# Kernel tuning notes

Hardware: AMD Instinct MI355X
Metric: run time of the kernel (lower is better)

Reference implementation:

```python
import jax, jax.numpy as jnp
import numpy as np

EPS = 1e-5
K = 7            # involution kernel size
GC = 16          # group_channels (involution default)
RED = 4          # reduction ratio (involution default)


def _bn(x, g, b, m, v):
    # eval-mode BatchNorm2d over channel dim of NCHW
    scale = g / jnp.sqrt(v + EPS)
    return x * scale[None, :, None, None] + (b - m * scale)[None, :, None, None]


def setup_inputs() -> dict:
    key = jax.random.key(0)
    ks = jax.random.split(key, 24)
    C_in, C_out = 64, 128
    B, H, W = 4, 96, 96
    G = C_in // GC          # 4 involution groups
    Cr = C_in // RED        # 16 reduced channels

    def bn_params(k, c):
        k1, k2, k3, k4 = jax.random.split(k, 4)
        return (jax.random.uniform(k1, (c,)) + 0.5,          # gamma
                jax.random.normal(k2, (c,)) * 0.1,            # beta
                jax.random.normal(k3, (c,)) * 0.1,            # running mean
                jax.random.uniform(k4, (c,)) + 0.5)           # running var

    g_r, b_r, m_r, v_r = bn_params(ks[1], Cr)
    g_i, b_i, m_i, v_i = bn_params(ks[2], C_in)
    g_c, b_c, m_c, v_c = bn_params(ks[3], C_out)
    g_m, b_m, m_m, v_m = bn_params(ks[4], C_out)

    return {
        "x": jax.random.normal(ks[0], (B, C_in, H, W), dtype=jnp.float32),
        "w_reduce": jax.random.normal(ks[5], (Cr, C_in), dtype=jnp.float32) * 0.1,
        "g_r": g_r, "b_r": b_r, "m_r": m_r, "v_r": v_r,
        "w_span": jax.random.normal(ks[6], (K * K * G, Cr), dtype=jnp.float32) * 0.1,
        "b_span": jax.random.normal(ks[7], (K * K * G,), dtype=jnp.float32) * 0.1,
        "g_i": g_i, "b_i": b_i, "m_i": m_i, "v_i": v_i,
        "w_conv": jax.random.normal(ks[8], (C_out, C_in), dtype=jnp.float32) * 0.1,
        "g_c": g_c, "b_c": b_c, "m_c": m_c, "v_c": v_c,
        "w_map": jax.random.normal(ks[9], (C_out, C_in), dtype=jnp.float32) * 0.1,
        "b_map": jax.random.normal(ks[10], (C_out,), dtype=jnp.float32) * 0.1,
        "g_m": g_m, "b_m": b_m, "m_m": m_m, "v_m": v_m,
    }


def reference(x, w_reduce, g_r, b_r, m_r, v_r, w_span, b_span,
              g_i, b_i, m_i, v_i, w_conv, g_c, b_c, m_c, v_c,
              w_map, b_map, g_m, b_m, m_m, v_m):
    B, C, H, W = x.shape
    G = C // GC
    pad = (K - 1) // 2

    # --- Involution: dynamic per-pixel kernels ---
    t = jax.nn.relu(_bn(jnp.einsum('rc,bchw->brhw', w_reduce, x), g_r, b_r, m_r, v_r))
    kern = jnp.einsum('or,brhw->bohw', w_span, t) + b_span[None, :, None, None]
    kern = kern.reshape(B, G, 1, K * K, H, W)  # [B,G,1,KK,H,W]

    xp = jnp.pad(x, ((0, 0), (0, 0), (pad, pad), (pad, pad)))
    # unfold in torch (C, kh, kw) order: C slowest -> stack over kernel offsets
    patches = jnp.stack([xp[:, :, i:i + H, j:j + W]
                         for i in range(K) for j in range(K)], axis=2)  # [B,C,KK,H,W]
    patches = patches.reshape(B, G, GC, K * K, H, W)
    inv = (kern * patches).sum(axis=3).reshape(B, C, H, W)

    # --- BN + GELU, 1x1 conv + BN, mapping branch, residual + GELU ---
    x1 = jax.nn.gelu(_bn(inv, g_i, b_i, m_i, v_i), approximate=False)
    x1 = _bn(jnp.einsum('oc,bchw->bohw', w_conv, x1), g_c, b_c, m_c, v_c)
    xm = _bn(jnp.einsum('oc,bchw->bohw', w_map, x) + b_map[None, :, None, None],
             g_m, b_m, m_m, v_m)
    return jax.nn.gelu(x1 + xm, approximate=False)
```

## Files before the change

kernel.cpp:

```cpp
#include <hip/hip_runtime.h>
#include <hip/hip_bf16.h>
#include <math.h>

typedef __hip_bfloat16 bf16;
typedef __attribute__((ext_vector_type(8))) short v8s;
typedef __attribute__((ext_vector_type(4))) short v4s;
typedef __attribute__((ext_vector_type(4))) float v4f;

#define HD 96
#define WD 96
#define HW 9216
#define BATCH 4

#define OFF_WR    0
#define OFF_CR    1024
#define OFF_WSP   1040
#define OFF_BSP   4176
#define OFF_SI    4372
#define OFF_CI    4436
#define OFF_BIAS  4500
#define WFRAG_BYTE 18512
#define ZT_BYTE   51328

__device__ __forceinline__ float geluf(float v) {
    return 0.5f * v * (1.0f + erff(v * 0.7071067811865475f));
}

__global__ __launch_bounds__(256) void k_fold(
    const float* __restrict__ wred,
    const float* __restrict__ gr, const float* __restrict__ br,
    const float* __restrict__ mr, const float* __restrict__ vr,
    const float* __restrict__ wspan, const float* __restrict__ bspan,
    const float* __restrict__ gi, const float* __restrict__ bi,
    const float* __restrict__ mi, const float* __restrict__ vi,
    const float* __restrict__ wconv,
    const float* __restrict__ gc, const float* __restrict__ bc,
    const float* __restrict__ mc, const float* __restrict__ vc,
    const float* __restrict__ wmap, const float* __restrict__ bmap,
    const float* __restrict__ gm, const float* __restrict__ bm,
    const float* __restrict__ mmn, const float* __restrict__ vm,
    float* __restrict__ wsf, bf16* __restrict__ wfrag)
{
    const int gt = blockIdx.x * 256 + threadIdx.x;

    if (gt < 1024) {
        int r = gt >> 6;
        float sr = gr[r] * rsqrtf(vr[r] + 1e-5f);
        wsf[OFF_WR + gt] = sr * wred[gt];
    }
    if (gt < 16) {
        float sr = gr[gt] * rsqrtf(vr[gt] + 1e-5f);
        wsf[OFF_CR + gt] = br[gt] - mr[gt] * sr;
    }
    if (gt < 3136) wsf[OFF_WSP + gt] = wspan[gt];
    if (gt < 196)  wsf[OFF_BSP + gt] = bspan[gt];
    if (gt < 64) {
        float si = gi[gt] * rsqrtf(vi[gt] + 1e-5f);
        wsf[OFF_SI + gt] = si;
        wsf[OFF_CI + gt] = bi[gt] - mi[gt] * si;
    }
    if (gt < 128) {
        float sc = gc[gt] * rsqrtf(vc[gt] + 1e-5f);
        float sm = gm[gt] * rsqrtf(vm[gt] + 1e-5f);
        wsf[OFF_BIAS + gt] = (bc[gt] - mc[gt] * sc)
                           + sm * bmap[gt]
                           + (bm[gt] - mmn[gt] * sm);
    }
    {
        int j    = gt & 7;
        int lane = (gt >> 3) & 63;
        int ks   = (gt >> 9) & 3;
        int mt   = gt >> 11;
        int m = mt * 16 + (lane & 15);
        int k = ks * 32 + (lane >> 4) * 8 + j;
        float v;
        if (k < 64) {
            float sc = gc[m] * rsqrtf(vc[m] + 1e-5f);
            v = sc * wconv[m * 64 + k];
        } else {
            float sm = gm[m] * rsqrtf(vm[m] + 1e-5f);
            v = sm * wmap[m * 64 + (k - 64)];
        }
        wfrag[gt] = __float2bfloat16(v);
    }
}

__global__ __launch_bounds__(256) void k_inv2(
    const float* __restrict__ x, const float* __restrict__ wsf,
    bf16* __restrict__ zt)
{
    __shared__ float xs4[3136];
    __shared__ float ks[49 * 64];
    __shared__ float ts[64 * 17];

    const int tid = threadIdx.x;
    const int bz  = blockIdx.z;
    const int b   = bz >> 2, g = bz & 3;
    const int ty  = blockIdx.y * 8, tx = blockIdx.x * 8;

    const float* xb = x + (size_t)b * 64 * HW;

    for (int it = tid; it < 784; it += 256) {
        int qc = it / 196, pos = it % 196;
        int py = pos / 14, px = pos % 14;
        int gy = ty + py - 3, gx = tx + px - 3;
        v4f v = (v4f){0.f, 0.f, 0.f, 0.f};
        if (gy >= 0 && gy < HD && gx >= 0 && gx < WD) {
            const float* pp = xb + (size_t)(g * 16 + qc * 4) * HW + gy * WD + gx;
            v[0] = pp[0]; v[1] = pp[HW]; v[2] = pp[2 * HW]; v[3] = pp[3 * HW];
        }
        *(v4f*)&xs4[it * 4] = v;
    }

    const int p  = tid & 63;
    const int u  = __builtin_amdgcn_readfirstlane(tid >> 6);
    const int py0 = p >> 3, px0 = p & 7;
    const int hw  = (ty + py0) * WD + (tx + px0);

    float t4[4];
    #pragma unroll
    for (int r = 0; r < 4; ++r) t4[r] = wsf[OFF_CR + u * 4 + r];
    #pragma unroll 4
    for (int c = 0; c < 64; ++c) {
        float xc = xb[(size_t)c * HW + hw];
        #pragma unroll
        for (int r = 0; r < 4; ++r)
            t4[r] += wsf[OFF_WR + (u * 4 + r) * 64 + c] * xc;
    }
    #pragma unroll
    for (int r = 0; r < 4; ++r) ts[p * 17 + u * 4 + r] = fmaxf(t4[r], 0.0f);
    __syncthreads();

    float tr[16];
    #pragma unroll
    for (int r = 0; r < 16; ++r) tr[r] = ts[p * 17 + r];

    for (int kk = u; kk < 49; kk += 4) {
        int row = g * 49 + kk;
        float kv = wsf[OFF_BSP + row];
        #pragma unroll
        for (int r = 0; r < 16; ++r) kv += wsf[OFF_WSP + row * 16 + r] * tr[r];
        ks[kk * 64 + p] = kv;
    }
    __syncthreads();

    float acc[4] = {0.f, 0.f, 0.f, 0.f};
    #pragma unroll 1
    for (int i = 0; i < 7; ++i) {
        const int rowb = (py0 + i) * 14 + px0;
        #pragma unroll
        for (int j = 0; j < 7; ++j) {
            float kv = ks[(i * 7 + j) * 64 + p];
            v4f xv = *(const v4f*)&xs4[(u * 196 + rowb + j) * 4];
            acc[0] += kv * xv[0];
            acc[1] += kv * xv[1];
            acc[2] += kv * xv[2];
            acc[3] += kv * xv[3];
        }
    }

    const int c0 = g * 16 + u * 4;
    bf16* ztr = zt + ((size_t)b * HW + hw) * 128;

    v4s pk1;
    #pragma unroll
    for (int ci = 0; ci < 4; ++ci) {
        float v = acc[ci] * wsf[OFF_SI + c0 + ci] + wsf[OFF_CI + c0 + ci];
        pk1[ci] = (short)__bfloat16_as_ushort(__float2bfloat16(geluf(v)));
    }
    *(v4s*)&ztr[c0] = pk1;

    const int center = (py0 + 3) * 14 + (px0 + 3);
    v4f xc = *(const v4f*)&xs4[(u * 196 + center) * 4];
    v4s pk2;
    #pragma unroll
    for (int ci = 0; ci < 4; ++ci)
        pk2[ci] = (short)__bfloat16_as_ushort(__float2bfloat16(xc[ci]));
    *(v4s*)&ztr[64 + c0] = pk2;
}

__global__ __launch_bounds__(256) void k_out2(
    const bf16* __restrict__ zt, const float* __restrict__ wsf,
    const bf16* __restrict__ wfrag, float* __restrict__ out)
{
    const int tid  = threadIdx.x;
    const int lane = tid & 63;
    const int wv   = tid >> 6;
    const int n    = lane & 15;
    const int quad = lane >> 4;

    const int pxg = blockIdx.x * 64 + wv * 16 + n;
    const int b   = pxg / HW;
    const int hw  = pxg % HW;

    const v8s* zb = (const v8s*)(zt + (size_t)pxg * 128);
    v8s bfr[4];
    #pragma unroll
    for (int ks = 0; ks < 4; ++ks) bfr[ks] = zb[ks * 4 + quad];

    const v8s* wf = (const v8s*)wfrag;
    v4f acc[8];
    #pragma unroll
    for (int mt = 0; mt < 8; ++mt) acc[mt] = (v4f){0.f, 0.f, 0.f, 0.f};

    #pragma unroll
    for (int ks = 0; ks < 4; ++ks) {
        #pragma unroll
        for (int mt = 0; mt < 8; ++mt) {
            v8s afrag = wf[(mt * 4 + ks) * 64 + lane];
            acc[mt] = __builtin_amdgcn_mfma_f32_16x16x32_bf16(afrag, bfr[ks], acc[mt], 0, 0, 0);
        }
    }

    #pragma unroll
    for (int mt = 0; mt < 8; ++mt) {
        int m0 = mt * 16 + quad * 4;
        v4f bs = *(const v4f*)&wsf[OFF_BIAS + m0];
        #pragma unroll
        for (int reg = 0; reg < 4; ++reg) {
            float v = acc[mt][reg] + bs[reg];
            out[((size_t)(b * 128 + m0 + reg)) * HW + hw] = geluf(v);
        }
    }
}

extern "C" void kernel_launch(void* const* d_in, const int* in_sizes, int n_in,
                              void* d_out, int out_size, void* d_ws, size_t ws_size,
                              hipStream_t stream)
{
    const float* x     = (const float*)d_in[0];
    const float* wred  = (const float*)d_in[1];
    const float* gr    = (const float*)d_in[2];
    const float* br    = (const float*)d_in[3];
    const float* mr    = (const float*)d_in[4];
    const float* vr    = (const float*)d_in[5];
    const float* wspan = (const float*)d_in[6];
    const float* bspan = (const float*)d_in[7];
    const float* gi    = (const float*)d_in[8];
    const float* bi    = (const float*)d_in[9];
    const float* mi    = (const float*)d_in[10];
    const float* vi    = (const float*)d_in[11];
    const float* wconv = (const float*)d_in[12];
    const float* gc    = (const float*)d_in[13];
    const float* bc    = (const float*)d_in[14];
    const float* mc    = (const float*)d_in[15];
    const float* vc    = (const float*)d_in[16];
    const float* wmap  = (const float*)d_in[17];
    const float* bmap  = (const float*)d_in[18];
    const float* gm    = (const float*)d_in[19];
    const float* bm    = (const float*)d_in[20];
    const float* mmn   = (const float*)d_in[21];
    const float* vm    = (const float*)d_in[22];

    float* wsf   = (float*)d_ws;
    bf16*  wfrag = (bf16*)((char*)d_ws + WFRAG_BYTE);
    bf16*  zt    = (bf16*)((char*)d_ws + ZT_BYTE);
    float* out   = (float*)d_out;

    hipLaunchKernelGGL(k_fold, dim3(64), dim3(256), 0, stream,
                       wred, gr, br, mr, vr, wspan, bspan, gi, bi, mi, vi,
                       wconv, gc, bc, mc, vc, wmap, bmap, gm, bm, mmn, vm,
                       wsf, wfrag);
    hipLaunchKernelGGL(k_inv2, dim3(12, 12, 16), dim3(256), 0, stream, x, wsf, zt);
    hipLaunchKernelGGL(k_out2, dim3((BATCH * HW) / 64), dim3(256), 0, stream,
                       zt, wsf, wfrag, out);
}
```

Measured before the change: 159.2 us.

## Fuse involution and output GEMM into one kernel with bf16 LDS halo

Merges the involution kernel and the MFMA output kernel into a single kernel, so each block handles a 16x4 pixel tile across all 4 groups and keeps the bf16 intermediate in shared memory. This removes the global round-trip of the 128-channel intermediate and one launch. The input halo for all 64 channels is now stored in LDS as bf16, which cuts LDS footprint but rounds the input to bf16 before the reduce conv and the involution. The grid shrinks to 576 blocks, each with more serialized work and more syncs, and the 16-wide tile has a larger halo overhead.

```diff
diff --git a/kernel.cpp b/kernel.cpp
--- a/kernel.cpp
+++ b/kernel.cpp
@@ -11,6 +11,13 @@
 #define WD 96
 #define HW 9216
 #define BATCH 4
+
+#define TW 16
+#define TH 4
+#define HALO_W 22
+#define HALO_H 10
+#define NPOS 220
+#define ZLS 136
 
 #define OFF_WR    0
 #define OFF_CR    1024
@@ -20,10 +27,21 @@
 #define OFF_CI    4436
 #define OFF_BIAS  4500
 #define WFRAG_BYTE 18512
-#define ZT_BYTE   51328
 
 __device__ __forceinline__ float geluf(float v) {
     return 0.5f * v * (1.0f + erff(v * 0.7071067811865475f));
+}
+__device__ __forceinline__ v4f up4(v4s s) {
+    v4f r;
+    #pragma unroll
+    for (int i = 0; i < 4; ++i) {
+        unsigned int uu = ((unsigned int)(unsigned short)s[i]) << 16;
+        r[i] = __builtin_bit_cast(float, uu);
+    }
+    return r;
+}
+__device__ __forceinline__ short pkbf(float f) {
+    return (short)__bfloat16_as_ushort(__float2bfloat16(f));
 }
 
 __global__ __launch_bounds__(256) void k_fold(
@@ -85,140 +103,140 @@
     }
 }
 
-__global__ __launch_bounds__(256) void k_inv2(
+__global__ __launch_bounds__(256) void k_main(
     const float* __restrict__ x, const float* __restrict__ wsf,
-    bf16* __restrict__ zt)
+    const bf16* __restrict__ wfrag, float* __restrict__ out)
 {
-    __shared__ float xs4[3136];
-    __shared__ float ks[49 * 64];
+    __shared__ v4s   xh4[16 * NPOS];
+    __shared__ float ksh[49 * 64];
     __shared__ float ts[64 * 17];
+    __shared__ short zl[64 * ZLS];
 
     const int tid = threadIdx.x;
-    const int bz  = blockIdx.z;
-    const int b   = bz >> 2, g = bz & 3;
-    const int ty  = blockIdx.y * 8, tx = blockIdx.x * 8;
+    const int b   = blockIdx.z;
+    const int ty  = blockIdx.y * TH;
+    const int tx  = blockIdx.x * TW;
 
     const float* xb = x + (size_t)b * 64 * HW;
 
-    for (int it = tid; it < 784; it += 256) {
-        int qc = it / 196, pos = it % 196;
-        int py = pos / 14, px = pos % 14;
+    for (int it = tid; it < 16 * NPOS; it += 256) {
+        int cb = it / NPOS, pos = it % NPOS;
+        int py = pos / HALO_W, px = pos % HALO_W;
         int gy = ty + py - 3, gx = tx + px - 3;
-        v4f v = (v4f){0.f, 0.f, 0.f, 0.f};
+        v4s v = (v4s){0, 0, 0, 0};
         if (gy >= 0 && gy < HD && gx >= 0 && gx < WD) {
-            const float* pp = xb + (size_t)(g * 16 + qc * 4) * HW + gy * WD + gx;
-            v[0] = pp[0]; v[1] = pp[HW]; v[2] = pp[2 * HW]; v[3] = pp[3 * HW];
-        }
-        *(v4f*)&xs4[it * 4] = v;
-    }
+            const float* pp = xb + (size_t)(cb * 4) * HW + gy * WD + gx;
+            v[0] = pkbf(pp[0]);
+            v[1] = pkbf(pp[HW]);
+            v[2] = pkbf(pp[2 * HW]);
+            v[3] = pkbf(pp[3 * HW]);
+        }
+        xh4[it] = v;
+    }
+    __syncthreads();
 
     const int p  = tid & 63;
     const int u  = __builtin_amdgcn_readfirstlane(tid >> 6);
-    const int py0 = p >> 3, px0 = p & 7;
-    const int hw  = (ty + py0) * WD + (tx + px0);
+    const int py0 = p >> 4, px0 = p & 15;
+    const int center = (py0 + 3) * HALO_W + (px0 + 3);
 
     float t4[4];
     #pragma unroll
     for (int r = 0; r < 4; ++r) t4[r] = wsf[OFF_CR + u * 4 + r];
-    #pragma unroll 4
-    for (int c = 0; c < 64; ++c) {
-        float xc = xb[(size_t)c * HW + hw];
-        #pragma unroll
-        for (int r = 0; r < 4; ++r)
-            t4[r] += wsf[OFF_WR + (u * 4 + r) * 64 + c] * xc;
+    #pragma unroll
+    for (int cb = 0; cb < 16; ++cb) {
+        v4f xf = up4(xh4[cb * NPOS + center]);
+        #pragma unroll
+        for (int ci = 0; ci < 4; ++ci) {
+            #pragma unroll
+            for (int r = 0; r < 4; ++r)
+                t4[r] += wsf[OFF_WR + (u * 4 + r) * 64 + cb * 4 + ci] * xf[ci];
+        }
     }
     #pragma unroll
     for (int r = 0; r < 4; ++r) ts[p * 17 + u * 4 + r] = fmaxf(t4[r], 0.0f);
+
+    #pragma unroll
+    for (int m = 0; m < 4; ++m) {
+        int cb = m * 4 + u;
+        *(v4s*)&zl[p * ZLS + 64 + cb * 4] = xh4[cb * NPOS + center];
+    }
     __syncthreads();
 
     float tr[16];
     #pragma unroll
     for (int r = 0; r < 16; ++r) tr[r] = ts[p * 17 + r];
 
-    for (int kk = u; kk < 49; kk += 4) {
-        int row = g * 49 + kk;
-        float kv = wsf[OFF_BSP + row];
-        #pragma unroll
-        for (int r = 0; r < 16; ++r) kv += wsf[OFF_WSP + row * 16 + r] * tr[r];
-        ks[kk * 64 + p] = kv;
-    }
-    __syncthreads();
-
-    float acc[4] = {0.f, 0.f, 0.f, 0.f};
-    #pragma unroll 1
-    for (int i = 0; i < 7; ++i) {
-        const int rowb = (py0 + i) * 14 + px0;
-        #pragma unroll
-        for (int j = 0; j < 7; ++j) {
-            float kv = ks[(i * 7 + j) * 64 + p];
-            v4f xv = *(const v4f*)&xs4[(u * 196 + rowb + j) * 4];
-            acc[0] += kv * xv[0];
-            acc[1] += kv * xv[1];
-            acc[2] += kv * xv[2];
-            acc[3] += kv * xv[3];
-        }
-    }
-
-    const int c0 = g * 16 + u * 4;
-    bf16* ztr = zt + ((size_t)b * HW + hw) * 128;
-
-    v4s pk1;
-    #pragma unroll
-    for (int ci = 0; ci < 4; ++ci) {
-        float v = acc[ci] * wsf[OFF_SI + c0 + ci] + wsf[OFF_CI + c0 + ci];
-        pk1[ci] = (short)__bfloat16_as_ushort(__float2bfloat16(geluf(v)));
-    }
-    *(v4s*)&ztr[c0] = pk1;
-
-    const int center = (py0 + 3) * 14 + (px0 + 3);
-    v4f xc = *(const v4f*)&xs4[(u * 196 + center) * 4];
-    v4s pk2;
-    #pragma unroll
-    for (int ci = 0; ci < 4; ++ci)
-        pk2[ci] = (short)__bfloat16_as_ushort(__float2bfloat16(xc[ci]));
-    *(v4s*)&ztr[64 + c0] = pk2;
-}
-
-__global__ __launch_bounds__(256) void k_out2(
-    const bf16* __restrict__ zt, const float* __restrict__ wsf,
-    const bf16* __restrict__ wfrag, float* __restrict__ out)
-{
-    const int tid  = threadIdx.x;
+    for (int g = 0; g < 4; ++g) {
+        for (int kk = u; kk < 49; kk += 4) {
+            int row = g * 49 + kk;
+            float kv = wsf[OFF_BSP + row];
+            #pragma unroll
+            for (int r = 0; r < 16; ++r) kv += wsf[OFF_WSP + row * 16 + r] * tr[r];
+            ksh[kk * 64 + p] = kv;
+        }
+        __syncthreads();
+
+        const int cb = g * 4 + u;
+        float acc[4] = {0.f, 0.f, 0.f, 0.f};
+        #pragma unroll 1
+        for (int i = 0; i < 7; ++i) {
+            const int rowb = (py0 + i) * HALO_W + px0;
+            #pragma unroll
+            for (int j = 0; j < 7; ++j) {
+                float kv = ksh[(i * 7 + j) * 64 + p];
+                v4f xv = up4(xh4[cb * NPOS + rowb + j]);
+                acc[0] += kv * xv[0];
+                acc[1] += kv * xv[1];
+                acc[2] += kv * xv[2];
+                acc[3] += kv * xv[3];
+            }
+        }
+
+        const int c0 = cb * 4;
+        v4s pk;
+        #pragma unroll
+        for (int ci = 0; ci < 4; ++ci) {
+            float v = acc[ci] * wsf[OFF_SI + c0 + ci] + wsf[OFF_CI + c0 + ci];
+            pk[ci] = pkbf(geluf(v));
+        }
+        *(v4s*)&zl[p * ZLS + c0] = pk;
+        __syncthreads();
+    }
+
     const int lane = tid & 63;
-    const int wv   = tid >> 6;
     const int n    = lane & 15;
     const int quad = lane >> 4;
-
-    const int pxg = blockIdx.x * 64 + wv * 16 + n;
-    const int b   = pxg / HW;
-    const int hw  = pxg % HW;
-
-    const v8s* zb = (const v8s*)(zt + (size_t)pxg * 128);
+    const int wv   = tid >> 6;
+    const int pxl  = wv * 16 + n;
+
     v8s bfr[4];
     #pragma unroll
-    for (int ks = 0; ks < 4; ++ks) bfr[ks] = zb[ks * 4 + quad];
+    for (int ki = 0; ki < 4; ++ki)
+        bfr[ki] = *(const v8s*)&zl[pxl * ZLS + ki * 32 + quad * 8];
 
     const v8s* wf = (const v8s*)wfrag;
-    v4f acc[8];
-    #pragma unroll
-    for (int mt = 0; mt < 8; ++mt) acc[mt] = (v4f){0.f, 0.f, 0.f, 0.f};
-
-    #pragma unroll
-    for (int ks = 0; ks < 4; ++ks) {
+    v4f acc2[8];
+    #pragma unroll
+    for (int mt = 0; mt < 8; ++mt) acc2[mt] = (v4f){0.f, 0.f, 0.f, 0.f};
+
+    #pragma unroll
+    for (int ki = 0; ki < 4; ++ki) {
         #pragma unroll
         for (int mt = 0; mt < 8; ++mt) {
-            v8s afrag = wf[(mt * 4 + ks) * 64 + lane];
-            acc[mt] = __builtin_amdgcn_mfma_f32_16x16x32_bf16(afrag, bfr[ks], acc[mt], 0, 0, 0);
-        }
-    }
-
+            v8s afrag = wf[(mt * 4 + ki) * 64 + lane];
+            acc2[mt] = __builtin_amdgcn_mfma_f32_16x16x32_bf16(afrag, bfr[ki], acc2[mt], 0, 0, 0);
+        }
+    }
+
+    const int hw = (ty + wv) * WD + tx + n;
     #pragma unroll
     for (int mt = 0; mt < 8; ++mt) {
         int m0 = mt * 16 + quad * 4;
         v4f bs = *(const v4f*)&wsf[OFF_BIAS + m0];
         #pragma unroll
         for (int reg = 0; reg < 4; ++reg) {
-            float v = acc[mt][reg] + bs[reg];
+            float v = acc2[mt][reg] + bs[reg];
             out[((size_t)(b * 128 + m0 + reg)) * HW + hw] = geluf(v);
         }
     }
@@ -254,14 +272,12 @@
 
     float* wsf   = (float*)d_ws;
     bf16*  wfrag = (bf16*)((char*)d_ws + WFRAG_BYTE);
-    bf16*  zt    = (bf16*)((char*)d_ws + ZT_BYTE);
     float* out   = (float*)d_out;
 
     hipLaunchKernelGGL(k_fold, dim3(64), dim3(256), 0, stream,
                        wred, gr, br, mr, vr, wspan, bspan, gi, bi, mi, vi,
                        wconv, gc, bc, mc, vc, wmap, bmap, gm, bm, mmn, vm,
                        wsf, wfrag);
-    hipLaunchKernelGGL(k_inv2, dim3(12, 12, 16), dim3(256), 0, stream, x, wsf, zt);
-    hipLaunchKernelGGL(k_out2, dim3((BATCH * HW) / 64), dim3(256), 0, stream,
-                       zt, wsf, wfrag, out);
-}
+    hipLaunchKernelGGL(k_main, dim3(WD / TW, HD / TH, BATCH), dim3(256), 0, stream,
+                       x, wsf, wfrag, out);
+}
```

Result: slower. 180.3 us (+13.2%).

## Precompute reduce-conv activations once per pixel and split output GEMM across waves

Applied to the files above, without the earlier changes.

The reduce 1x1 conv (64->16 channels plus BN and ReLU) was previously recomputed in every involution block, once for each of the 4 groups. It is now computed once per pixel in a new stage fused into the weight-folding kernel and stored as bf16. The involution kernel reads these 16 values instead of re-reading all 64 input channels. The output kernel now gives each wave 2 of the 8 M-tiles for 16 pixels instead of all 8 tiles for its own pixels, which means more blocks and fewer accumulators per thread. The cost is an extra bf16 round trip through global memory and a small loss of precision on the reduced activations.

```diff
diff --git a/kernel.cpp b/kernel.cpp
--- a/kernel.cpp
+++ b/kernel.cpp
@@ -11,6 +11,7 @@
 #define WD 96
 #define HW 9216
 #define BATCH 4
+#define NPIX (BATCH * HW)
 
 #define OFF_WR    0
 #define OFF_CR    1024
@@ -20,13 +21,22 @@
 #define OFF_CI    4436
 #define OFF_BIAS  4500
 #define WFRAG_BYTE 18512
-#define ZT_BYTE   51328
+#define TG_BYTE   51328
+#define ZT_BYTE   1230976
 
 __device__ __forceinline__ float geluf(float v) {
     return 0.5f * v * (1.0f + erff(v * 0.7071067811865475f));
 }
-
-__global__ __launch_bounds__(256) void k_fold(
+__device__ __forceinline__ float upbf(short s) {
+    unsigned int uu = ((unsigned int)(unsigned short)s) << 16;
+    return __builtin_bit_cast(float, uu);
+}
+__device__ __forceinline__ short pkbf(float f) {
+    return (short)__bfloat16_as_ushort(__float2bfloat16(f));
+}
+
+__global__ __launch_bounds__(256) void k_pre(
+    const float* __restrict__ x,
     const float* __restrict__ wred,
     const float* __restrict__ gr, const float* __restrict__ br,
     const float* __restrict__ mr, const float* __restrict__ vr,
@@ -39,59 +49,98 @@
     const float* __restrict__ wmap, const float* __restrict__ bmap,
     const float* __restrict__ gm, const float* __restrict__ bm,
     const float* __restrict__ mmn, const float* __restrict__ vm,
-    float* __restrict__ wsf, bf16* __restrict__ wfrag)
+    float* __restrict__ wsf, bf16* __restrict__ wfrag, bf16* __restrict__ tg)
 {
-    const int gt = blockIdx.x * 256 + threadIdx.x;
-
-    if (gt < 1024) {
-        int r = gt >> 6;
-        float sr = gr[r] * rsqrtf(vr[r] + 1e-5f);
-        wsf[OFF_WR + gt] = sr * wred[gt];
-    }
-    if (gt < 16) {
-        float sr = gr[gt] * rsqrtf(vr[gt] + 1e-5f);
-        wsf[OFF_CR + gt] = br[gt] - mr[gt] * sr;
-    }
-    if (gt < 3136) wsf[OFF_WSP + gt] = wspan[gt];
-    if (gt < 196)  wsf[OFF_BSP + gt] = bspan[gt];
-    if (gt < 64) {
-        float si = gi[gt] * rsqrtf(vi[gt] + 1e-5f);
-        wsf[OFF_SI + gt] = si;
-        wsf[OFF_CI + gt] = bi[gt] - mi[gt] * si;
-    }
-    if (gt < 128) {
-        float sc = gc[gt] * rsqrtf(vc[gt] + 1e-5f);
-        float sm = gm[gt] * rsqrtf(vm[gt] + 1e-5f);
-        wsf[OFF_BIAS + gt] = (bc[gt] - mc[gt] * sc)
-                           + sm * bmap[gt]
-                           + (bm[gt] - mmn[gt] * sm);
-    }
-    {
-        int j    = gt & 7;
-        int lane = (gt >> 3) & 63;
-        int ks   = (gt >> 9) & 3;
-        int mt   = gt >> 11;
-        int m = mt * 16 + (lane & 15);
-        int k = ks * 32 + (lane >> 4) * 8 + j;
-        float v;
-        if (k < 64) {
-            float sc = gc[m] * rsqrtf(vc[m] + 1e-5f);
-            v = sc * wconv[m * 64 + k];
-        } else {
-            float sm = gm[m] * rsqrtf(vm[m] + 1e-5f);
-            v = sm * wmap[m * 64 + (k - 64)];
-        }
-        wfrag[gt] = __float2bfloat16(v);
-    }
-}
-
-__global__ __launch_bounds__(256) void k_inv2(
+    const int tid = threadIdx.x;
+    const int blk = blockIdx.x;
+
+    if (blk < 64) {
+        const int gt = blk * 256 + tid;
+        if (gt < 1024) {
+            int r = gt >> 6;
+            float sr = gr[r] * rsqrtf(vr[r] + 1e-5f);
+            wsf[OFF_WR + gt] = sr * wred[gt];
+        }
+        if (gt < 16) {
+            float sr = gr[gt] * rsqrtf(vr[gt] + 1e-5f);
+            wsf[OFF_CR + gt] = br[gt] - mr[gt] * sr;
+        }
+        if (gt < 3136) wsf[OFF_WSP + gt] = wspan[gt];
+        if (gt < 196)  wsf[OFF_BSP + gt] = bspan[gt];
+        if (gt < 64) {
+            float si = gi[gt] * rsqrtf(vi[gt] + 1e-5f);
+            wsf[OFF_SI + gt] = si;
+            wsf[OFF_CI + gt] = bi[gt] - mi[gt] * si;
+        }
+        if (gt < 128) {
+            float sc = gc[gt] * rsqrtf(vc[gt] + 1e-5f);
+            float sm = gm[gt] * rsqrtf(vm[gt] + 1e-5f);
+            wsf[OFF_BIAS + gt] = (bc[gt] - mc[gt] * sc)
+                               + sm * bmap[gt]
+                               + (bm[gt] - mmn[gt] * sm);
+        }
+        {
+            int j    = gt & 7;
+            int lane = (gt >> 3) & 63;
+            int ks   = (gt >> 9) & 3;
+            int mt   = gt >> 11;
+            int m = mt * 16 + (lane & 15);
+            int k = ks * 32 + (lane >> 4) * 8 + j;
+            float v;
+            if (k < 64) {
+                float sc = gc[m] * rsqrtf(vc[m] + 1e-5f);
+                v = sc * wconv[m * 64 + k];
+            } else {
+                float sm = gm[m] * rsqrtf(vm[m] + 1e-5f);
+                v = sm * wmap[m * 64 + (k - 64)];
+            }
+            wfrag[gt] = __float2bfloat16(v);
+        }
+        return;
+    }
+
+    __shared__ float wrl[1024];
+    __shared__ float crl[16];
+    for (int i = tid; i < 1024; i += 256) {
+        int r = i >> 6;
+        wrl[i] = gr[r] * rsqrtf(vr[r] + 1e-5f) * wred[i];
+    }
+    if (tid < 16)
+        crl[tid] = br[tid] - mr[tid] * gr[tid] * rsqrtf(vr[tid] + 1e-5f);
+    __syncthreads();
+
+    const int p = tid & 63, u = tid >> 6;
+    const int gpix = (blk - 64) * 64 + p;
+    const int b = gpix / HW, hw = gpix % HW;
+    const float* xb = x + (size_t)b * 64 * HW + hw;
+
+    float t4[4];
+    #pragma unroll
+    for (int r = 0; r < 4; ++r) t4[r] = crl[u * 4 + r];
+    #pragma unroll 4
+    for (int c4 = 0; c4 < 16; ++c4) {
+        float xc0 = xb[(size_t)(c4 * 4 + 0) * HW];
+        float xc1 = xb[(size_t)(c4 * 4 + 1) * HW];
+        float xc2 = xb[(size_t)(c4 * 4 + 2) * HW];
+        float xc3 = xb[(size_t)(c4 * 4 + 3) * HW];
+        #pragma unroll
+        for (int r = 0; r < 4; ++r) {
+            v4f w = *(const v4f*)&wrl[(u * 4 + r) * 64 + c4 * 4];
+            t4[r] += w[0] * xc0 + w[1] * xc1 + w[2] * xc2 + w[3] * xc3;
+        }
+    }
+    v4s pk;
+    #pragma unroll
+    for (int r = 0; r < 4; ++r) pk[r] = pkbf(fmaxf(t4[r], 0.0f));
+    *(v4s*)((short*)tg + (size_t)gpix * 16 + u * 4) = pk;
+}
+
+__global__ __launch_bounds__(256) void k_inv3(
     const float* __restrict__ x, const float* __restrict__ wsf,
-    bf16* __restrict__ zt)
+    const bf16* __restrict__ tg, bf16* __restrict__ zt)
 {
     __shared__ float xs4[3136];
-    __shared__ float ks[49 * 64];
-    __shared__ float ts[64 * 17];
+    __shared__ float ksh[49 * 64];
 
     const int tid = threadIdx.x;
     const int bz  = blockIdx.z;
@@ -116,31 +165,20 @@
     const int u  = __builtin_amdgcn_readfirstlane(tid >> 6);
     const int py0 = p >> 3, px0 = p & 7;
     const int hw  = (ty + py0) * WD + (tx + px0);
-
-    float t4[4];
-    #pragma unroll
-    for (int r = 0; r < 4; ++r) t4[r] = wsf[OFF_CR + u * 4 + r];
-    #pragma unroll 4
-    for (int c = 0; c < 64; ++c) {
-        float xc = xb[(size_t)c * HW + hw];
-        #pragma unroll
-        for (int r = 0; r < 4; ++r)
-            t4[r] += wsf[OFF_WR + (u * 4 + r) * 64 + c] * xc;
-    }
-    #pragma unroll
-    for (int r = 0; r < 4; ++r) ts[p * 17 + u * 4 + r] = fmaxf(t4[r], 0.0f);
-    __syncthreads();
-
+    const int gpix = b * HW + hw;
+
+    const v8s* tp = (const v8s*)((const short*)tg + (size_t)gpix * 16);
+    v8s t01 = tp[0], t23 = tp[1];
     float tr[16];
     #pragma unroll
-    for (int r = 0; r < 16; ++r) tr[r] = ts[p * 17 + r];
+    for (int i = 0; i < 8; ++i) { tr[i] = upbf(t01[i]); tr[8 + i] = upbf(t23[i]); }
 
     for (int kk = u; kk < 49; kk += 4) {
         int row = g * 49 + kk;
         float kv = wsf[OFF_BSP + row];
         #pragma unroll
         for (int r = 0; r < 16; ++r) kv += wsf[OFF_WSP + row * 16 + r] * tr[r];
-        ks[kk * 64 + p] = kv;
+        ksh[kk * 64 + p] = kv;
     }
     __syncthreads();
 
@@ -150,7 +188,7 @@
         const int rowb = (py0 + i) * 14 + px0;
         #pragma unroll
         for (int j = 0; j < 7; ++j) {
-            float kv = ks[(i * 7 + j) * 64 + p];
+            float kv = ksh[(i * 7 + j) * 64 + p];
             v4f xv = *(const v4f*)&xs4[(u * 196 + rowb + j) * 4];
             acc[0] += kv * xv[0];
             acc[1] += kv * xv[1];
@@ -166,7 +204,7 @@
     #pragma unroll
     for (int ci = 0; ci < 4; ++ci) {
         float v = acc[ci] * wsf[OFF_SI + c0 + ci] + wsf[OFF_CI + c0 + ci];
-        pk1[ci] = (short)__bfloat16_as_ushort(__float2bfloat16(geluf(v)));
+        pk1[ci] = pkbf(geluf(v));
     }
     *(v4s*)&ztr[c0] = pk1;
 
@@ -174,51 +212,51 @@
     v4f xc = *(const v4f*)&xs4[(u * 196 + center) * 4];
     v4s pk2;
     #pragma unroll
-    for (int ci = 0; ci < 4; ++ci)
-        pk2[ci] = (short)__bfloat16_as_ushort(__float2bfloat16(xc[ci]));
+    for (int ci = 0; ci < 4; ++ci) pk2[ci] = pkbf(xc[ci]);
     *(v4s*)&ztr[64 + c0] = pk2;
 }
 
-__global__ __launch_bounds__(256) void k_out2(
+__global__ __launch_bounds__(256) void k_out3(
     const bf16* __restrict__ zt, const float* __restrict__ wsf,
     const bf16* __restrict__ wfrag, float* __restrict__ out)
 {
     const int tid  = threadIdx.x;
     const int lane = tid & 63;
-    const int wv   = tid >> 6;
+    const int mq   = tid >> 6;
     const int n    = lane & 15;
     const int quad = lane >> 4;
 
-    const int pxg = blockIdx.x * 64 + wv * 16 + n;
+    const int pxg = blockIdx.x * 16 + n;
     const int b   = pxg / HW;
     const int hw  = pxg % HW;
 
     const v8s* zb = (const v8s*)(zt + (size_t)pxg * 128);
     v8s bfr[4];
     #pragma unroll
-    for (int ks = 0; ks < 4; ++ks) bfr[ks] = zb[ks * 4 + quad];
+    for (int ki = 0; ki < 4; ++ki) bfr[ki] = zb[ki * 4 + quad];
 
     const v8s* wf = (const v8s*)wfrag;
-    v4f acc[8];
-    #pragma unroll
-    for (int mt = 0; mt < 8; ++mt) acc[mt] = (v4f){0.f, 0.f, 0.f, 0.f};
-
-    #pragma unroll
-    for (int ks = 0; ks < 4; ++ks) {
-        #pragma unroll
-        for (int mt = 0; mt < 8; ++mt) {
-            v8s afrag = wf[(mt * 4 + ks) * 64 + lane];
-            acc[mt] = __builtin_amdgcn_mfma_f32_16x16x32_bf16(afrag, bfr[ks], acc[mt], 0, 0, 0);
-        }
-    }
-
-    #pragma unroll
-    for (int mt = 0; mt < 8; ++mt) {
-        int m0 = mt * 16 + quad * 4;
+    v4f acc[2];
+    acc[0] = (v4f){0.f, 0.f, 0.f, 0.f};
+    acc[1] = (v4f){0.f, 0.f, 0.f, 0.f};
+
+    #pragma unroll
+    for (int ki = 0; ki < 4; ++ki) {
+        #pragma unroll
+        for (int m = 0; m < 2; ++m) {
+            int mt = mq * 2 + m;
+            v8s afrag = wf[(mt * 4 + ki) * 64 + lane];
+            acc[m] = __builtin_amdgcn_mfma_f32_16x16x32_bf16(afrag, bfr[ki], acc[m], 0, 0, 0);
+        }
+    }
+
+    #pragma unroll
+    for (int m = 0; m < 2; ++m) {
+        int m0 = (mq * 2 + m) * 16 + quad * 4;
         v4f bs = *(const v4f*)&wsf[OFF_BIAS + m0];
         #pragma unroll
         for (int reg = 0; reg < 4; ++reg) {
-            float v = acc[mt][reg] + bs[reg];
+            float v = acc[m][reg] + bs[reg];
             out[((size_t)(b * 128 + m0 + reg)) * HW + hw] = geluf(v);
         }
     }
@@ -254,14 +292,16 @@
 
     float* wsf   = (float*)d_ws;
     bf16*  wfrag = (bf16*)((char*)d_ws + WFRAG_BYTE);
+    bf16*  tg    = (bf16*)((char*)d_ws + TG_BYTE);
     bf16*  zt    = (bf16*)((char*)d_ws + ZT_BYTE);
     float* out   = (float*)d_out;
 
-    hipLaunchKernelGGL(k_fold, dim3(64), dim3(256), 0, stream,
-                       wred, gr, br, mr, vr, wspan, bspan, gi, bi, mi, vi,
+    hipLaunchKernelGGL(k_pre, dim3(64 + NPIX / 64), dim3(256), 0, stream,
+                       x, wred, gr, br, mr, vr, wspan, bspan, gi, bi, mi, vi,
                        wconv, gc, bc, mc, vc, wmap, bmap, gm, bm, mmn, vm,
-                       wsf, wfrag);
-    hipLaunchKernelGGL(k_inv2, dim3(12, 12, 16), dim3(256), 0, stream, x, wsf, zt);
-    hipLaunchKernelGGL(k_out2, dim3((BATCH * HW) / 64), dim3(256), 0, stream,
+                       wsf, wfrag, tg);
+    hipLaunchKernelGGL(k_inv3, dim3(12, 12, 16), dim3(256), 0, stream,
+                       x, wsf, tg, zt);
+    hipLaunchKernelGGL(k_out3, dim3(NPIX / 16), dim3(256), 0, stream,
                        zt, wsf, wfrag, out);
 }
```

New measurement: 145.1 us. 8.9% less time.
